# Performance work log

Hardware: AMD Instinct MI355X
Metric: run time of the kernel (lower is better)

The kernel has to match this reference:

```python
import jax, jax.numpy as jnp
from jax import lax
import numpy as np

B, S, H = 8, 512, 768


def setup_inputs() -> dict:
    key = jax.random.key(0)
    ks = jax.random.split(key, 8)
    outputs = jax.random.normal(ks[0], (B, S, H), dtype=jnp.float32)
    starts = jax.random.randint(ks[1], (B,), S // 4, 3 * S // 4)
    mask = jnp.stack([starts, jnp.full((B,), S, dtype=starts.dtype)], axis=1)  # [B,2]
    sc = 1.0 / np.sqrt(H)
    Wa_w = jax.random.normal(ks[2], (H, H), dtype=jnp.float32) * sc
    Wa_b = jax.random.normal(ks[3], (H,), dtype=jnp.float32) * sc
    Ua_w = jax.random.normal(ks[4], (H, H), dtype=jnp.float32) * sc
    Ua_b = jax.random.normal(ks[5], (H,), dtype=jnp.float32) * sc
    Va_w = jax.random.normal(ks[6], (1, H), dtype=jnp.float32) * sc
    Va_b = jax.random.normal(ks[7], (1,), dtype=jnp.float32) * sc
    return {"outputs": outputs, "mask": mask, "Wa_w": Wa_w, "Wa_b": Wa_b,
            "Ua_w": Ua_w, "Ua_b": Ua_b, "Va_w": Va_w, "Va_b": Va_b}


def reference(outputs, mask, Wa_w, Wa_b, Ua_w, Ua_b, Va_w, Va_b):
    # outputs: [B,S,H]; mask[:,0] = start (source = tokens [0:start], summary = [start:S])
    b, s, h = outputs.shape
    Wq = jnp.einsum('bsh,oh->bso', outputs, Wa_w) + Wa_b  # query proj, [B,S,H]
    Uk = jnp.einsum('bsh,oh->bso', outputs, Ua_w) + Ua_b  # key proj,   [B,S,H]
    va = Va_w[0]  # [H]
    vb = Va_b[0]

    # Stream over query token positions to avoid a [B,S,S,H] tanh intermediate.
    def step(_, wq_t):  # wq_t: [B,H]
        m = jnp.tanh(wq_t[:, None, :] + Uk)          # [B,S,H]
        sc_t = jnp.einsum('bkh,h->bk', m, va) + vb   # [B,S]
        return None, sc_t

    _, scores = lax.scan(step, None, jnp.swapaxes(Wq, 0, 1))  # [S(query token), B, S(key)]
    scores = jnp.swapaxes(scores, 0, 1)  # [B, S_token, S_key]

    start = mask[:, 0]                              # [B]
    j = jnp.arange(s)
    # summary query j corresponds to token index start + j
    t_idx = jnp.clip(start[:, None] + j[None, :], 0, s - 1)            # [B,S]
    sc = jnp.take_along_axis(scores, t_idx[:, :, None], axis=1)       # [B,S,S]
    key_mask = (j[None, :] < start[:, None])                           # [B,S] valid source keys
    q_mask = (j[None, :] < (s - start)[:, None])                       # [B,S] valid summary queries

    sc = jnp.where(key_mask[:, None, :], sc, -1e30)
    w = jax.nn.softmax(sc, axis=-1)
    # zero out exactly where the torch code leaves zeros
    attentions = w * key_mask[:, None, :].astype(w.dtype) * q_mask[:, :, None].astype(w.dtype)
    contexts = jnp.einsum('bjk,bkh->bjh', attentions, outputs)
    return attentions, contexts
```

## Files before the change

### kernel.cpp

```cpp
#include <hip/hip_runtime.h>

typedef float  f32x4   __attribute__((ext_vector_type(4)));
typedef short  short8  __attribute__((ext_vector_type(8)));
typedef unsigned short ushort8 __attribute__((ext_vector_type(8)));

constexpr int kB = 8;
constexpr int kS = 512;
constexpr int kH = 768;
constexpr int kJM = 384;

constexpr float kTanhScale = 2.8853900817779268f;

__device__ __forceinline__ float native_exp2(float x) {
    float r; asm("v_exp_f32 %0, %1" : "=v"(r) : "v"(x)); return r;
}

__device__ __forceinline__ unsigned short bf16_rtn(float x) {
    unsigned u = __float_as_uint(x);
    unsigned r = u + 0x7FFFu + ((u >> 16) & 1u);
    return (unsigned short)(r >> 16);
}

__device__ __forceinline__ float waveMax(float v) {
#pragma unroll
    for (int off = 32; off > 0; off >>= 1) v = fmaxf(v, __shfl_xor(v, off, 64));
    return v;
}
__device__ __forceinline__ float waveSum(float v) {
#pragma unroll
    for (int off = 32; off > 0; off >>= 1) v += __shfl_xor(v, off, 64);
    return v;
}

__global__ __launch_bounds__(256) void k0_convert(
    const float* __restrict__ X, const float* __restrict__ Wa, const float* __restrict__ Ua,
    unsigned short* __restrict__ Xhi, unsigned short* __restrict__ Xlo,
    unsigned short* __restrict__ Wahi, unsigned short* __restrict__ Uahi)
{
    const int i4 = blockIdx.x * 256 + threadIdx.x;
    if (i4 < 786432) {
        float4 v = *(const float4*)(X + (size_t)i4 * 4);
        unsigned short h[4], l[4];
#pragma unroll
        for (int c = 0; c < 4; ++c) {
            float x = (&v.x)[c];
            h[c] = bf16_rtn(x);
            float hf = __uint_as_float((unsigned)h[c] << 16);
            l[c] = bf16_rtn(x - hf);
        }
        *(ushort4*)(Xhi + (size_t)i4 * 4) = make_ushort4(h[0], h[1], h[2], h[3]);
        *(ushort4*)(Xlo + (size_t)i4 * 4) = make_ushort4(l[0], l[1], l[2], l[3]);
    } else {
        const float* src; unsigned short* hi; int off;
        if (i4 < 933888) { src = Wa; hi = Wahi; off = i4 - 786432; }
        else             { src = Ua; hi = Uahi; off = i4 - 933888; }
        float4 v = *(const float4*)(src + (size_t)off * 4);
        *(ushort4*)(hi + (size_t)off * 4) =
            make_ushort4(bf16_rtn(v.x), bf16_rtn(v.y), bf16_rtn(v.z), bf16_rtn(v.w));
    }
}

__global__ __launch_bounds__(256) void k1_mfma(
    const unsigned short* __restrict__ Xhi, const unsigned short* __restrict__ Xlo,
    const unsigned short* __restrict__ W0hi, const unsigned short* __restrict__ W1hi,
    const float* __restrict__ b0, const float* __restrict__ b1,
    const int* __restrict__ mask,
    float* __restrict__ Eqc, float* __restrict__ EkTc)
{
    __shared__ char smem[49664];
    unsigned short* Ahi = (unsigned short*)smem;
    unsigned short* Alo = (unsigned short*)(smem + 10240);
    unsigned short* Bhi = (unsigned short*)(smem + 20480);

    const int z = blockIdx.z;
    const unsigned short* Whi = z ? W1hi : W0hi;
    const float* bias = z ? b1 : b0;

    const int m0 = blockIdx.y * 128;
    const int n0 = blockIdx.x * 96;
    const int t  = threadIdx.x;
    const int bI = m0 >> 9;
    const int lb = m0 & (kS - 1);
    const int start = mask[2 * bI];

    if (z == 0) { if (lb + 128 <= start) return; }
    else        { if (lb >= start) return; }

    const int ar = t >> 1, ko = (t & 1) << 4;
    const bool doB = (ar < 96);
    const size_t aoff = (size_t)(m0 + ar) * kH + ko;
    const size_t woff = (size_t)(n0 + ar) * kH + ko;

    const int wid = t >> 6, lane = t & 63;
    const int wr = wid >> 1, wc = wid & 1;
    const int lr = lane & 15, lk = (lane >> 4) << 3;

    f32x4 acc[4][3];
#pragma unroll
    for (int mi = 0; mi < 4; ++mi)
#pragma unroll
        for (int ni = 0; ni < 3; ++ni)
#pragma unroll
            for (int r = 0; r < 4; ++r) acc[mi][ni][r] = 0.0f;

    for (int h0 = 0; h0 < kH; h0 += 32) {
        ushort8 ah0 = *(const ushort8*)(Xhi + aoff + h0);
        ushort8 ah1 = *(const ushort8*)(Xhi + aoff + h0 + 8);
        ushort8 al0 = *(const ushort8*)(Xlo + aoff + h0);
        ushort8 al1 = *(const ushort8*)(Xlo + aoff + h0 + 8);
        ushort8 bh0, bh1;
        if (doB) {
            bh0 = *(const ushort8*)(Whi + woff + h0);
            bh1 = *(const ushort8*)(Whi + woff + h0 + 8);
        }
        __syncthreads();
        *(ushort8*)(Ahi + ar * 40 + ko)     = ah0;
        *(ushort8*)(Ahi + ar * 40 + ko + 8) = ah1;
        *(ushort8*)(Alo + ar * 40 + ko)     = al0;
        *(ushort8*)(Alo + ar * 40 + ko + 8) = al1;
        if (doB) {
            *(ushort8*)(Bhi + ar * 40 + ko)     = bh0;
            *(ushort8*)(Bhi + ar * 40 + ko + 8) = bh1;
        }
        __syncthreads();

        short8 ah[4], al_[4], bh[3];
#pragma unroll
        for (int mi = 0; mi < 4; ++mi) {
            const int row = wr * 64 + mi * 16 + lr;
            ah[mi]  = *(const short8*)(Ahi + row * 40 + lk);
            al_[mi] = *(const short8*)(Alo + row * 40 + lk);
        }
#pragma unroll
        for (int ni = 0; ni < 3; ++ni) {
            const int row = wc * 48 + ni * 16 + lr;
            bh[ni] = *(const short8*)(Bhi + row * 40 + lk);
        }
#pragma unroll
        for (int mi = 0; mi < 4; ++mi)
#pragma unroll
            for (int ni = 0; ni < 3; ++ni)
                acc[mi][ni] = __builtin_amdgcn_mfma_f32_16x16x32_bf16(ah[mi], bh[ni], acc[mi][ni], 0, 0, 0);
#pragma unroll
        for (int mi = 0; mi < 4; ++mi)
#pragma unroll
            for (int ni = 0; ni < 3; ++ni)
                acc[mi][ni] = __builtin_amdgcn_mfma_f32_16x16x32_bf16(al_[mi], bh[ni], acc[mi][ni], 0, 0, 0);
    }

    if (z == 0) {
#pragma unroll
        for (int mi = 0; mi < 4; ++mi)
#pragma unroll
            for (int ni = 0; ni < 3; ++ni) {
                const int ml = lb + wr * 64 + mi * 16 + ((lane >> 4) << 2);
                const int ng = n0 + wc * 48 + ni * 16 + lr;
                const float bn = bias[ng];
#pragma unroll
                for (int r = 0; r < 4; ++r) {
                    const int jj = ml + r - start;
                    if (jj >= 0)
                        Eqc[((size_t)bI * kJM + jj) * kH + ng] =
                            native_exp2((acc[mi][ni][r] + bn) * kTanhScale);
                }
            }
    } else {
        __syncthreads();
        float* stg = (float*)smem;
#pragma unroll
        for (int mi = 0; mi < 4; ++mi)
#pragma unroll
            for (int ni = 0; ni < 3; ++ni) {
                const int ml = wr * 64 + mi * 16 + ((lane >> 4) << 2);
                const int nl = wc * 48 + ni * 16 + lr;
                const float bn = bias[n0 + nl];
#pragma unroll
                for (int r = 0; r < 4; ++r)
                    stg[(ml + r) * 97 + nl] = native_exp2((acc[mi][ni][r] + bn) * kTanhScale);
            }
        __syncthreads();
        const int s4 = (t & 31) << 2, hb_ = t >> 5;
        const int sg = lb + s4;
#pragma unroll
        for (int u = 0; u < 12; ++u) {
            const int h = (u << 3) + hb_;
            float o[4] = { stg[(s4 + 0) * 97 + h], stg[(s4 + 1) * 97 + h],
                           stg[(s4 + 2) * 97 + h], stg[(s4 + 3) * 97 + h] };
            float* dst = EkTc + ((size_t)bI * kH + n0 + h) * kJM + sg;
            if (sg + 3 < start) {
                *(float4*)dst = make_float4(o[0], o[1], o[2], o[3]);
            } else {
#pragma unroll
                for (int e2 = 0; e2 < 4; ++e2)
                    if (sg + e2 < start) dst[e2] = o[e2];
            }
        }
    }
}

__global__ void k2a_worklist(const int* __restrict__ mask, int* __restrict__ wl)
{
    __shared__ int ne[kB], off[kB];
    const int tid = threadIdx.x;
    if (tid < kB) {
        int start = mask[2 * tid];
        ne[tid] = ((kS - start + 3) >> 2) * ((start + 63) >> 6) * 2;
    }
    __syncthreads();
    if (tid == 0) {
        int s = 0;
        for (int b = 0; b < kB; ++b) { off[b] = s; s += ne[b]; }
        wl[0] = s;
    }
    __syncthreads();
    for (int b = 0; b < kB; ++b) {
        int start = mask[2 * b];
        int nkw = (start + 63) >> 6;
        int nkc = nkw * 2;
        int n = ne[b], base = off[b];
        for (int t = tid; t < n; t += blockDim.x) {
            int jt = t / nkc;
            int r = t - jt * nkc;
            int kt = r >> 1, c = r & 1;
            wl[1 + base + t] = (b << 16) | (jt << 8) | (kt << 1) | c;
        }
    }
}

__global__ __launch_bounds__(256) void k2_scores(
    const float* __restrict__ Eqc, const float* __restrict__ EkTc,
    const float* __restrict__ va, const int* __restrict__ mask,
    const int* __restrict__ wl, float* __restrict__ part0, float* __restrict__ part1)
{
    constexpr int JT = 4;
    const int ntiles = wl[0];
    const int lane = threadIdx.x & 63;
    const int wslot = (blockIdx.x << 2) | (threadIdx.x >> 6);
    const int nslots = gridDim.x << 2;

    for (int w = wslot; w < ntiles; w += nslots) {
        const int e = __builtin_amdgcn_readfirstlane(wl[1 + w]);
        const int b = e >> 16, jt = (e >> 8) & 255, ktc = e & 255;
        const int kt = ktc >> 1, c = ktc & 1;
        const int start = __builtin_amdgcn_readfirstlane(mask[2 * b]);
        const int jmax = kS - start;
        const int j0 = jt * JT, k0 = kt << 6;
        const int hbase = c * 384;

        const float* eqr[JT];
#pragma unroll
        for (int j = 0; j < JT; ++j)
            eqr[j] = Eqc + ((size_t)b * kJM + j0 + j) * kH + hbase;
        const float* ekp = EkTc + ((size_t)b * kH + hbase) * kJM + k0 + lane;
        const float* vap = va + hbase;

        float acc[JT] = {};
        float eA[8], eB[8];
#pragma unroll
        for (int c2 = 0; c2 < 8; ++c2) eA[c2] = ekp[(size_t)c2 * kJM];
#pragma unroll
        for (int c2 = 0; c2 < 8; ++c2) eB[c2] = ekp[(size_t)(8 + c2) * kJM];

        for (int h0 = 0; h0 < 384; h0 += 16) {
            const bool more = (h0 + 16) < 384;
            float nA[8], nB[8];
            if (more) {
#pragma unroll
                for (int c2 = 0; c2 < 8; ++c2) nA[c2] = ekp[(size_t)(h0 + 16 + c2) * kJM];
            }
#pragma unroll
            for (int c2 = 0; c2 < 8; ++c2) {
                const float vc = vap[h0 + c2];
#pragma unroll
                for (int j = 0; j < JT; ++j) {
                    float r = __builtin_amdgcn_rcpf(fmaf(eqr[j][h0 + c2], eA[c2], 1.0f));
                    acc[j] = fmaf(vc, r, acc[j]);
                }
            }
            if (more) {
#pragma unroll
                for (int c2 = 0; c2 < 8; ++c2) nB[c2] = ekp[(size_t)(h0 + 24 + c2) * kJM];
            }
#pragma unroll
            for (int c2 = 0; c2 < 8; ++c2) {
                const float vc = vap[h0 + 8 + c2];
#pragma unroll
                for (int j = 0; j < JT; ++j) {
                    float r = __builtin_amdgcn_rcpf(fmaf(eqr[j][h0 + 8 + c2], eB[c2], 1.0f));
                    acc[j] = fmaf(vc, r, acc[j]);
                }
            }
            if (more) {
#pragma unroll
                for (int c2 = 0; c2 < 8; ++c2) { eA[c2] = nA[c2]; eB[c2] = nB[c2]; }
            }
        }

        float* srow = (c ? part1 : part0) + ((size_t)b * kS + j0) * kS + k0 + lane;
#pragma unroll
        for (int j = 0; j < JT; ++j)
            if (j0 + j < jmax) srow[(size_t)j * kS] = -2.0f * acc[j];
    }
}

__global__ __launch_bounds__(256) void k4a_convert(
    const float* __restrict__ X,
    unsigned short* __restrict__ OThi, unsigned short* __restrict__ OTlo)
{
    __shared__ float st[64][65];
    const int b = blockIdx.z;
    const int s0 = blockIdx.y * 64;
    const int h0 = blockIdx.x * 64;
    const int t = threadIdx.x;

    const int sr = t >> 2, hc = (t & 3) << 4;
    const float* src = X + ((size_t)b * kS + s0 + sr) * kH + h0 + hc;
#pragma unroll
    for (int q = 0; q < 4; ++q) {
        float4 v = *(const float4*)(src + 4 * q);
        st[sr][hc + 4 * q + 0] = v.x;
        st[sr][hc + 4 * q + 1] = v.y;
        st[sr][hc + 4 * q + 2] = v.z;
        st[sr][hc + 4 * q + 3] = v.w;
    }
    __syncthreads();

    const int hr = t >> 2, sc = (t & 3) << 4;
    unsigned short h[16], l[16];
#pragma unroll
    for (int i = 0; i < 16; ++i) {
        float x = st[sc + i][hr];
        h[i] = bf16_rtn(x);
        float hf = __uint_as_float((unsigned)h[i] << 16);
        l[i] = bf16_rtn(x - hf);
    }
    const size_t dst = ((size_t)b * kH + h0 + hr) * kJM + s0 + sc;
    *(ushort8*)(OThi + dst)     = *(ushort8*)(h);
    *(ushort8*)(OThi + dst + 8) = *(ushort8*)(h + 8);
    *(ushort8*)(OTlo + dst)     = *(ushort8*)(l);
    *(ushort8*)(OTlo + dst + 8) = *(ushort8*)(l + 8);
}

__global__ __launch_bounds__(256) void k3_softmax(
    float* __restrict__ attn, const float* __restrict__ part1,
    const int* __restrict__ mask,
    unsigned short* __restrict__ Ahi, unsigned short* __restrict__ Alo)
{
    const int bx = blockIdx.x;
    const int b = bx >> 9;
    const int j = bx & (kS - 1);
    const int start = mask[2 * b];
    float* row = attn + ((size_t)b * kS + j) * kS;
    const int tid = threadIdx.x;
    const size_t abase = ((size_t)b * kS + j) * kJM;

    if (j >= kS - start) {
        row[tid] = 0.0f;
        row[tid + 256] = 0.0f;
        Ahi[abase + tid] = 0; Alo[abase + tid] = 0;
        if (tid < 128) { Ahi[abase + 256 + tid] = 0; Alo[abase + 256 + tid] = 0; }
        return;
    }

    const float* p1row = part1 + ((size_t)b * kS + j) * kS;
    float v0 = (tid < start) ? row[tid] + p1row[tid] : -1e30f;
    float v1 = (tid + 256 < start) ? row[tid + 256] + p1row[tid + 256] : -1e30f;

    __shared__ float red[4];
    const int wid = tid >> 6;

    float m = waveMax(fmaxf(v0, v1));
    if ((tid & 63) == 0) red[wid] = m;
    __syncthreads();
    m = fmaxf(fmaxf(red[0], red[1]), fmaxf(red[2], red[3]));
    __syncthreads();

    float e0 = (tid < start) ? __expf(v0 - m) : 0.0f;
    float e1 = (tid + 256 < start) ? __expf(v1 - m) : 0.0f;
    float s = waveSum(e0 + e1);
    if ((tid & 63) == 0) red[wid] = s;
    __syncthreads();
    s = red[0] + red[1] + red[2] + red[3];

    float inv = __builtin_amdgcn_rcpf(s);
    float a0 = e0 * inv, a1 = e1 * inv;
    row[tid] = a0;
    row[tid + 256] = a1;

    unsigned short h0 = bf16_rtn(a0);
    Ahi[abase + tid] = h0;
    Alo[abase + tid] = bf16_rtn(a0 - __uint_as_float((unsigned)h0 << 16));
    if (tid < 128) {
        unsigned short h1 = bf16_rtn(a1);
        Ahi[abase + 256 + tid] = h1;
        Alo[abase + 256 + tid] = bf16_rtn(a1 - __uint_as_float((unsigned)h1 << 16));
    }
}

__global__ __launch_bounds__(256) void k4_mfma(
    const unsigned short* __restrict__ Ahi_g, const unsigned short* __restrict__ Alo_g,
    const unsigned short* __restrict__ Bhi_g, const unsigned short* __restrict__ Blo_g,
    const int* __restrict__ mask, float* __restrict__ ctx)
{
    __shared__ char smem[35840];
    unsigned short* Ahi = (unsigned short*)smem;
    unsigned short* Alo = (unsigned short*)(smem + 10240);
    unsigned short* Bhi = (unsigned short*)(smem + 20480);
    unsigned short* Blo = (unsigned short*)(smem + 28160);

    const int m0 = blockIdx.y * 128;
    const int n0 = blockIdx.x * 96;
    const int t  = threadIdx.x;
    const int bI = m0 >> 9;
    const int jb = m0 & (kS - 1);
    const int start = mask[2 * bI];
    const int kmax = (start + 31) & ~31;

    const int ar = t >> 1, ko = (t & 1) << 4;
    const bool doB = (ar < 96);
    const size_t aoff = ((size_t)bI * kS + jb + ar) * kJM + ko;
    const size_t woff = ((size_t)bI * kH + n0 + ar) * kJM + ko;

    const int wid = t >> 6, lane = t & 63;
    const int wr = wid >> 1, wc = wid & 1;
    const int lr = lane & 15, lk = (lane >> 4) << 3;

    f32x4 acc[4][3];
#pragma unroll
    for (int mi = 0; mi < 4; ++mi)
#pragma unroll
        for (int ni = 0; ni < 3; ++ni)
#pragma unroll
            for (int r = 0; r < 4; ++r) acc[mi][ni][r] = 0.0f;

    for (int k0 = 0; k0 < kmax; k0 += 32) {
        ushort8 ah0 = *(const ushort8*)(Ahi_g + aoff + k0);
        ushort8 ah1 = *(const ushort8*)(Ahi_g + aoff + k0 + 8);
        ushort8 al0 = *(const ushort8*)(Alo_g + aoff + k0);
        ushort8 al1 = *(const ushort8*)(Alo_g + aoff + k0 + 8);
        ushort8 bh0, bh1, bl0, bl1;
        if (doB) {
            bh0 = *(const ushort8*)(Bhi_g + woff + k0);
            bh1 = *(const ushort8*)(Bhi_g + woff + k0 + 8);
            bl0 = *(const ushort8*)(Blo_g + woff + k0);
            bl1 = *(const ushort8*)(Blo_g + woff + k0 + 8);
        }
        __syncthreads();
        *(ushort8*)(Ahi + ar * 40 + ko)     = ah0;
        *(ushort8*)(Ahi + ar * 40 + ko + 8) = ah1;
        *(ushort8*)(Alo + ar * 40 + ko)     = al0;
        *(ushort8*)(Alo + ar * 40 + ko + 8) = al1;
        if (doB) {
            *(ushort8*)(Bhi + ar * 40 + ko)     = bh0;
            *(ushort8*)(Bhi + ar * 40 + ko + 8) = bh1;
            *(ushort8*)(Blo + ar * 40 + ko)     = bl0;
            *(ushort8*)(Blo + ar * 40 + ko + 8) = bl1;
        }
        __syncthreads();

        short8 ah[4], al_[4], bh[3], bl[3];
#pragma unroll
        for (int mi = 0; mi < 4; ++mi) {
            const int row = wr * 64 + mi * 16 + lr;
            ah[mi]  = *(const short8*)(Ahi + row * 40 + lk);
            al_[mi] = *(const short8*)(Alo + row * 40 + lk);
        }
#pragma unroll
        for (int ni = 0; ni < 3; ++ni) {
            const int row = wc * 48 + ni * 16 + lr;
            bh[ni] = *(const short8*)(Bhi + row * 40 + lk);
            bl[ni] = *(const short8*)(Blo + row * 40 + lk);
        }
#pragma unroll
        for (int mi = 0; mi < 4; ++mi)
#pragma unroll
            for (int ni = 0; ni < 3; ++ni)
                acc[mi][ni] = __builtin_amdgcn_mfma_f32_16x16x32_bf16(ah[mi], bh[ni], acc[mi][ni], 0, 0, 0);
#pragma unroll
        for (int mi = 0; mi < 4; ++mi)
#pragma unroll
            for (int ni = 0; ni < 3; ++ni)
                acc[mi][ni] = __builtin_amdgcn_mfma_f32_16x16x32_bf16(al_[mi], bh[ni], acc[mi][ni], 0, 0, 0);
#pragma unroll
        for (int mi = 0; mi < 4; ++mi)
#pragma unroll
            for (int ni = 0; ni < 3; ++ni)
                acc[mi][ni] = __builtin_amdgcn_mfma_f32_16x16x32_bf16(ah[mi], bl[ni], acc[mi][ni], 0, 0, 0);
    }

#pragma unroll
    for (int mi = 0; mi < 4; ++mi)
#pragma unroll
        for (int ni = 0; ni < 3; ++ni) {
            const int mg = m0 + wr * 64 + mi * 16 + ((lane >> 4) << 2);
            const int ng = n0 + wc * 48 + ni * 16 + lr;
#pragma unroll
            for (int r = 0; r < 4; ++r)
                ctx[(size_t)(mg + r) * kH + ng] = acc[mi][ni][r];
        }
}

extern "C" void kernel_launch(void* const* d_in, const int* in_sizes, int n_in,
                              void* d_out, int out_size, void* d_ws, size_t ws_size,
                              hipStream_t stream)
{
    const float* outputs = (const float*)d_in[0];
    const int*   mask    = (const int*)d_in[1];
    const float* Wa_w    = (const float*)d_in[2];
    const float* Wa_b    = (const float*)d_in[3];
    const float* Ua_w    = (const float*)d_in[4];
    const float* Ua_b    = (const float*)d_in[5];
    const float* Va_w    = (const float*)d_in[6];

    float* attn = (float*)d_out;
    float* ctx  = attn + (size_t)kB * kS * kS;

    unsigned short* Xhi  = (unsigned short*)ctx;
    unsigned short* Xlo  = Xhi + (size_t)kB * kS * kH;
    unsigned short* Wahi = (unsigned short*)attn;
    unsigned short* Uahi = Wahi + (size_t)kH * kH;
    float* part1 = ctx;

    int* wl = (int*)d_ws;
    float* Eqc  = (float*)((char*)d_ws + 131072);
    float* EkTc = Eqc + (size_t)kB * kJM * kH;

    unsigned short* AttnHi = (unsigned short*)Eqc;
    unsigned short* AttnLo = AttnHi + (size_t)kB * kS * kJM;
    unsigned short* OThi   = (unsigned short*)EkTc;
    unsigned short* OTlo   = OThi + (size_t)kB * kH * kJM;

    k0_convert<<<dim3(4224), 256, 0, stream>>>(
        outputs, Wa_w, Ua_w, Xhi, Xlo, Wahi, Uahi);

    k1_mfma<<<dim3(kH / 96, (kB * kS) / 128, 2), 256, 0, stream>>>(
        Xhi, Xlo, Wahi, Uahi, Wa_b, Ua_b, mask, Eqc, EkTc);

    k2a_worklist<<<dim3(1), 256, 0, stream>>>(mask, wl);
    k2_scores<<<dim3(2048), 256, 0, stream>>>(Eqc, EkTc, Va_w, mask, wl, attn, part1);

    k4a_convert<<<dim3(kH / 64, kJM / 64, kB), 256, 0, stream>>>(outputs, OThi, OTlo);

    k3_softmax<<<dim3(kB * kS), 256, 0, stream>>>(attn, part1, mask, AttnHi, AttnLo);

    k4_mfma<<<dim3(kH / 96, (kB * kS) / 128), 256, 0, stream>>>(
        AttnHi, AttnLo, OThi, OTlo, mask, ctx);
}
```

Baseline: 146.6 us.

## Tile key projection layout by 64-key blocks and compute worklist inline

The transposed key projection is now stored in 64-key tiles ([b][kt][h][64]), so each wave's strided loads in the scores kernel walk a compact 256-byte row stride instead of a full 384-key stride. The separate single-block worklist kernel is removed; each wave now rebuilds its tile assignment from the mask with a few scalar ops, saving a launch and a global indirection. The inline decode adds a division and a per-batch scan to each iteration.

```diff
diff --git a/kernel.cpp b/kernel.cpp
--- a/kernel.cpp
+++ b/kernel.cpp
@@ -65,7 +65,7 @@
     const unsigned short* __restrict__ W0hi, const unsigned short* __restrict__ W1hi,
     const float* __restrict__ b0, const float* __restrict__ b1,
     const int* __restrict__ mask,
-    float* __restrict__ Eqc, float* __restrict__ EkTc)
+    float* __restrict__ Eqc, float* __restrict__ Ek2)
 {
     __shared__ char smem[49664];
     unsigned short* Ahi = (unsigned short*)smem;
@@ -186,7 +186,7 @@
             const int h = (u << 3) + hb_;
             float o[4] = { stg[(s4 + 0) * 97 + h], stg[(s4 + 1) * 97 + h],
                            stg[(s4 + 2) * 97 + h], stg[(s4 + 3) * 97 + h] };
-            float* dst = EkTc + ((size_t)bI * kH + n0 + h) * kJM + sg;
+            float* dst = Ek2 + (((size_t)bI * 6 + (sg >> 6)) * kH + n0 + h) * 64 + (sg & 63);
             if (sg + 3 < start) {
                 *(float4*)dst = make_float4(o[0], o[1], o[2], o[3]);
             } else {
@@ -198,52 +198,38 @@
     }
 }
 
-__global__ void k2a_worklist(const int* __restrict__ mask, int* __restrict__ wl)
-{
-    __shared__ int ne[kB], off[kB];
-    const int tid = threadIdx.x;
-    if (tid < kB) {
-        int start = mask[2 * tid];
-        ne[tid] = ((kS - start + 3) >> 2) * ((start + 63) >> 6) * 2;
-    }
-    __syncthreads();
-    if (tid == 0) {
-        int s = 0;
-        for (int b = 0; b < kB; ++b) { off[b] = s; s += ne[b]; }
-        wl[0] = s;
-    }
-    __syncthreads();
-    for (int b = 0; b < kB; ++b) {
-        int start = mask[2 * b];
-        int nkw = (start + 63) >> 6;
-        int nkc = nkw * 2;
-        int n = ne[b], base = off[b];
-        for (int t = tid; t < n; t += blockDim.x) {
-            int jt = t / nkc;
-            int r = t - jt * nkc;
-            int kt = r >> 1, c = r & 1;
-            wl[1 + base + t] = (b << 16) | (jt << 8) | (kt << 1) | c;
-        }
-    }
-}
-
 __global__ __launch_bounds__(256) void k2_scores(
-    const float* __restrict__ Eqc, const float* __restrict__ EkTc,
+    const float* __restrict__ Eqc, const float* __restrict__ Ek2,
     const float* __restrict__ va, const int* __restrict__ mask,
-    const int* __restrict__ wl, float* __restrict__ part0, float* __restrict__ part1)
+    float* __restrict__ part0, float* __restrict__ part1)
 {
     constexpr int JT = 4;
-    const int ntiles = wl[0];
     const int lane = threadIdx.x & 63;
     const int wslot = (blockIdx.x << 2) | (threadIdx.x >> 6);
     const int nslots = gridDim.x << 2;
 
+    int ne[kB];
+    int ntiles = 0;
+#pragma unroll
+    for (int i = 0; i < kB; ++i) {
+        int s = __builtin_amdgcn_readfirstlane(mask[2 * i]);
+        ne[i] = ((kS - s + 3) >> 2) * ((s + 63) >> 6) * 2;
+        ntiles += ne[i];
+    }
+
     for (int w = wslot; w < ntiles; w += nslots) {
-        const int e = __builtin_amdgcn_readfirstlane(wl[1 + w]);
-        const int b = e >> 16, jt = (e >> 8) & 255, ktc = e & 255;
-        const int kt = ktc >> 1, c = ktc & 1;
+        int rem = w, b = 0;
+#pragma unroll
+        for (int i = 0; i < kB - 1; ++i) {
+            bool go = (b == i) && (rem >= ne[i]);
+            if (go) { rem -= ne[i]; b = i + 1; }
+        }
         const int start = __builtin_amdgcn_readfirstlane(mask[2 * b]);
         const int jmax = kS - start;
+        const int nkc = ((start + 63) >> 6) << 1;
+        const int jt = rem / nkc;
+        const int r2 = rem - jt * nkc;
+        const int kt = r2 >> 1, c = r2 & 1;
         const int j0 = jt * JT, k0 = kt << 6;
         const int hbase = c * 384;
 
@@ -251,22 +237,22 @@
 #pragma unroll
         for (int j = 0; j < JT; ++j)
             eqr[j] = Eqc + ((size_t)b * kJM + j0 + j) * kH + hbase;
-        const float* ekp = EkTc + ((size_t)b * kH + hbase) * kJM + k0 + lane;
+        const float* ekp = Ek2 + (((size_t)b * 6 + kt) * kH + hbase) * 64 + lane;
         const float* vap = va + hbase;
 
         float acc[JT] = {};
         float eA[8], eB[8];
 #pragma unroll
-        for (int c2 = 0; c2 < 8; ++c2) eA[c2] = ekp[(size_t)c2 * kJM];
-#pragma unroll
-        for (int c2 = 0; c2 < 8; ++c2) eB[c2] = ekp[(size_t)(8 + c2) * kJM];
+        for (int c2 = 0; c2 < 8; ++c2) eA[c2] = ekp[(size_t)c2 * 64];
+#pragma unroll
+        for (int c2 = 0; c2 < 8; ++c2) eB[c2] = ekp[(size_t)(8 + c2) * 64];
 
         for (int h0 = 0; h0 < 384; h0 += 16) {
             const bool more = (h0 + 16) < 384;
             float nA[8], nB[8];
             if (more) {
 #pragma unroll
-                for (int c2 = 0; c2 < 8; ++c2) nA[c2] = ekp[(size_t)(h0 + 16 + c2) * kJM];
+                for (int c2 = 0; c2 < 8; ++c2) nA[c2] = ekp[(size_t)(h0 + 16 + c2) * 64];
             }
 #pragma unroll
             for (int c2 = 0; c2 < 8; ++c2) {
@@ -279,7 +265,7 @@
             }
             if (more) {
 #pragma unroll
-                for (int c2 = 0; c2 < 8; ++c2) nB[c2] = ekp[(size_t)(h0 + 24 + c2) * kJM];
+                for (int c2 = 0; c2 < 8; ++c2) nB[c2] = ekp[(size_t)(h0 + 24 + c2) * 64];
             }
 #pragma unroll
             for (int c2 = 0; c2 < 8; ++c2) {
@@ -521,23 +507,21 @@
     unsigned short* Uahi = Wahi + (size_t)kH * kH;
     float* part1 = ctx;
 
-    int* wl = (int*)d_ws;
-    float* Eqc  = (float*)((char*)d_ws + 131072);
-    float* EkTc = Eqc + (size_t)kB * kJM * kH;
+    float* Eqc = (float*)((char*)d_ws + 131072);
+    float* Ek2 = Eqc + (size_t)kB * kJM * kH;
 
     unsigned short* AttnHi = (unsigned short*)Eqc;
     unsigned short* AttnLo = AttnHi + (size_t)kB * kS * kJM;
-    unsigned short* OThi   = (unsigned short*)EkTc;
+    unsigned short* OThi   = (unsigned short*)Ek2;
     unsigned short* OTlo   = OThi + (size_t)kB * kH * kJM;
 
     k0_convert<<<dim3(4224), 256, 0, stream>>>(
         outputs, Wa_w, Ua_w, Xhi, Xlo, Wahi, Uahi);
 
     k1_mfma<<<dim3(kH / 96, (kB * kS) / 128, 2), 256, 0, stream>>>(
-        Xhi, Xlo, Wahi, Uahi, Wa_b, Ua_b, mask, Eqc, EkTc);
-
-    k2a_worklist<<<dim3(1), 256, 0, stream>>>(mask, wl);
-    k2_scores<<<dim3(2048), 256, 0, stream>>>(Eqc, EkTc, Va_w, mask, wl, attn, part1);
+        Xhi, Xlo, Wahi, Uahi, Wa_b, Ua_b, mask, Eqc, Ek2);
+
+    k2_scores<<<dim3(2048), 256, 0, stream>>>(Eqc, Ek2, Va_w, mask, attn, part1);
 
     k4a_convert<<<dim3(kH / 64, kJM / 64, kB), 256, 0, stream>>>(outputs, OThi, OTlo);
 
```

New measurement: 168.3 us. +14.8%, slower.
